# Kernel optimization log

Hardware: AMD Instinct MI355X
Metric: run time of the kernel (lower is better)

Reference implementation:

```python
import jax, jax.numpy as jnp
import numpy as np

T, B, E, H, PD, PV = 256, 64, 768, 512, 100, 1000
H2 = 2 * H


def setup_inputs() -> dict:
    key = jax.random.key(0)
    ks = jax.random.split(key, 20)
    sc_rnn = 1.0 / np.sqrt(H)
    sc_lin = 1.0 / np.sqrt(H2)
    n = lambda k, shape, s: (jax.random.normal(k, shape, jnp.float32) * s)
    return {
        "emb": n(ks[0], (T, B, E), 1.0),
        "lengths": jnp.full((B,), T, dtype=jnp.int32),
        # bidirectional LSTM params (PyTorch gate order i,f,g,o); b = b_ih + b_hh
        "w_ih_f": n(ks[1], (4 * H, E), sc_rnn),
        "w_hh_f": n(ks[2], (4 * H, H), sc_rnn),
        "b_f": n(ks[3], (4 * H,), sc_rnn),
        "w_ih_b": n(ks[4], (4 * H, E), sc_rnn),
        "w_hh_b": n(ks[5], (4 * H, H), sc_rnn),
        "b_b": n(ks[6], (4 * H,), sc_rnn),
        "W_fdoc": n(ks[7], (H2, H2), sc_lin),
        "b_fdoc": n(ks[8], (H2,), sc_lin),
        "pos_emb": n(ks[9], (PV, PD), 1.0),
        "w_content": n(ks[10], (H2,), sc_lin),
        "W_sal": n(ks[11], (H2, H2), sc_lin),
        "W_nov": n(ks[12], (H2, H2), sc_lin),
        "w_abs": n(ks[13], (PD,), 1.0 / np.sqrt(PD)),
        "bias": n(ks[14], (), 0.05),
    }


def _lstm_dir(x, w_ih, w_hh, b, reverse):
    # x: [T, B, E]; batch_first=True in the original means dim0 (T) is batch
    # and dim1 (B) is the scan (sequence) axis.
    pre = jnp.einsum('tbe,ge->tbg', x, w_ih) + b  # [T, B, 4H]
    if reverse:
        pre = pre[:, ::-1]
    pre_s = jnp.swapaxes(pre, 0, 1)  # [B, T, 4H] -> scan over B

    def step(carry, p):
        h, c = carry
        g = p + h @ w_hh.T
        i, f, gg, o = jnp.split(g, 4, axis=-1)
        c = jax.nn.sigmoid(f) * c + jax.nn.sigmoid(i) * jnp.tanh(gg)
        h = jax.nn.sigmoid(o) * jnp.tanh(c)
        return (h, c), h

    init = (jnp.zeros((x.shape[0], w_hh.shape[1]), x.dtype),
            jnp.zeros((x.shape[0], w_hh.shape[1]), x.dtype))
    _, hs = jax.lax.scan(step, init, pre_s)  # [B, T, H]
    hs = jnp.swapaxes(hs, 0, 1)  # [T, B, H]
    if reverse:
        hs = hs[:, ::-1]
    return hs


def reference(emb, lengths, w_ih_f, w_hh_f, b_f, w_ih_b, w_hh_b, b_b,
              W_fdoc, b_fdoc, pos_emb, w_content, W_sal, W_nov, w_abs, bias):
    # lengths are assumed full (= T) for static shapes under jit.
    del lengths
    fwd = _lstm_dir(emb, w_ih_f, w_hh_f, b_f, reverse=False)
    bwd = _lstm_dir(emb, w_ih_b, w_hh_b, b_b, reverse=True)
    sents = jnp.concatenate([fwd, bwd], axis=-1)  # [T, B, 2H]

    hsd = jnp.swapaxes(sents, 0, 1)  # [B, T, 2H] per-document hidden states
    doc = jnp.tanh(hsd.mean(axis=1) @ W_fdoc.T + b_fdoc)  # [B, 2H]

    cont = hsd @ w_content                                  # [B, T]
    sal = jnp.einsum('bth,hk,bk->bt', hsd, W_sal, doc)      # [B, T]
    abs_p = pos_emb[jnp.minimum(jnp.arange(T), PV - 1)] @ w_abs  # [T]
    s0 = cont + sal + abs_p[None, :] + bias                 # [B, T]

    # sequential summary recurrence over sentence positions, batched over docs
    xs = (jnp.swapaxes(hsd, 0, 1), s0.T)  # ([T,B,2H], [T,B])

    def step(summ, x):
        h, s = x
        nov = jnp.einsum('bh,hk,bk->b', h, W_nov, jnp.tanh(summ))
        prob = jax.nn.sigmoid(s - nov)
        summ = summ + prob[:, None] * h
        return summ, prob

    _, probs = jax.lax.scan(step, jnp.zeros((B, H2), emb.dtype), xs)  # [T, B]
    # original concatenates doc-by-doc, position-major within each doc
    return probs.T.reshape(-1)  # [B*T]
```

## Files before the change

### kernel.cpp

```cpp
#include <hip/hip_runtime.h>


typedef _Float16 f16x8 __attribute__((ext_vector_type(8)));
typedef float f32x4 __attribute__((ext_vector_type(4)));
typedef unsigned short us4 __attribute__((ext_vector_type(4)));
typedef unsigned short us8 __attribute__((ext_vector_type(8)));
typedef unsigned int u32x4 __attribute__((ext_vector_type(4)));

#define DEV __device__ __forceinline__

DEV unsigned short f2h(float f) {
  _Float16 h = (_Float16)f;
  return __builtin_bit_cast(unsigned short, h);
}
DEV float h2f(unsigned short u) {
  return (float)__builtin_bit_cast(_Float16, u);
}
DEV float sigf(float x) { return 1.f / (1.f + __expf(-x)); }
DEV float tanhf_(float x) { return 1.f - 2.f / (__expf(2.f * x) + 1.f); }

DEV void store_b64_llc(unsigned short* addr, us4 v) {
  asm volatile("global_store_dwordx2 %0, %1, off sc0 sc1" ::"v"(addr), "v"(v)
               : "memory");
}
DEV void waitcnt_vm0() { asm volatile("s_waitcnt vmcnt(0)" ::: "memory"); }

DEV void load_frags16_llc(const unsigned short* base, f16x8 af[16]) {
  asm volatile(
      "global_load_dwordx4 %0, %16, off sc0 sc1\n\t"
      "global_load_dwordx4 %1, %16, off offset:64 sc0 sc1\n\t"
      "global_load_dwordx4 %2, %16, off offset:128 sc0 sc1\n\t"
      "global_load_dwordx4 %3, %16, off offset:192 sc0 sc1\n\t"
      "global_load_dwordx4 %4, %16, off offset:256 sc0 sc1\n\t"
      "global_load_dwordx4 %5, %16, off offset:320 sc0 sc1\n\t"
      "global_load_dwordx4 %6, %16, off offset:384 sc0 sc1\n\t"
      "global_load_dwordx4 %7, %16, off offset:448 sc0 sc1\n\t"
      "global_load_dwordx4 %8, %16, off offset:512 sc0 sc1\n\t"
      "global_load_dwordx4 %9, %16, off offset:576 sc0 sc1\n\t"
      "global_load_dwordx4 %10, %16, off offset:640 sc0 sc1\n\t"
      "global_load_dwordx4 %11, %16, off offset:704 sc0 sc1\n\t"
      "global_load_dwordx4 %12, %16, off offset:768 sc0 sc1\n\t"
      "global_load_dwordx4 %13, %16, off offset:832 sc0 sc1\n\t"
      "global_load_dwordx4 %14, %16, off offset:896 sc0 sc1\n\t"
      "global_load_dwordx4 %15, %16, off offset:960 sc0 sc1\n\t"
      "s_waitcnt vmcnt(0)"
      : "=v"(af[0]), "=v"(af[1]), "=v"(af[2]), "=v"(af[3]), "=v"(af[4]),
        "=v"(af[5]), "=v"(af[6]), "=v"(af[7]), "=v"(af[8]), "=v"(af[9]),
        "=v"(af[10]), "=v"(af[11]), "=v"(af[12]), "=v"(af[13]), "=v"(af[14]),
        "=v"(af[15])
      : "v"(base)
      : "memory");
}

DEV void cvt4seg(const float* __restrict__ src, unsigned short* __restrict__ dst,
                 size_t nquads, size_t gt, size_t NT) {
  const f32x4* s4 = (const f32x4*)src;
  us4* d4 = (us4*)dst;
  for (size_t i = gt; i < nquads; i += NT) {
    f32x4 v = s4[i];
    us4 o = {f2h(v[0]), f2h(v[1]), f2h(v[2]), f2h(v[3])};
    d4[i] = o;
  }
}

__global__ __launch_bounds__(256, 1) void prep_kernel(
    const float* __restrict__ emb, const float* __restrict__ wihf,
    const float* __restrict__ whhf, const float* __restrict__ bf_,
    const float* __restrict__ wihb, const float* __restrict__ whhb,
    const float* __restrict__ bb_, const float* __restrict__ posemb,
    const float* __restrict__ Wnov, const float* __restrict__ wabs,
    unsigned short* __restrict__ emb_t, unsigned short* __restrict__ wcat,
    unsigned short* __restrict__ whh, unsigned short* __restrict__ WnT,
    float* __restrict__ bcat, float* __restrict__ absp,
    unsigned short* __restrict__ hst, int* __restrict__ cnt) {
  size_t gt = (size_t)blockIdx.x * 256 + threadIdx.x;
  size_t NT = (size_t)gridDim.x * 256;
  for (size_t i = gt; i < 3145728u; i += NT) {
    size_t r = i / 192, e4 = i % 192;
    size_t b = r >> 8, t = r & 255;
    f32x4 v = *(const f32x4*)(emb + (t * 64 + b) * 768 + e4 * 4);
    us4 o = {f2h(v[0]), f2h(v[1]), f2h(v[2]), f2h(v[3])};
    ((us4*)emb_t)[i] = o;
  }
  cvt4seg(wihf, wcat, 393216u, gt, NT);
  cvt4seg(wihb, wcat + 1572864, 393216u, gt, NT);
  cvt4seg(whhf, whh, 262144u, gt, NT);
  cvt4seg(whhb, whh + 1048576, 262144u, gt, NT);
  for (size_t i = gt; i < 1048576u; i += NT) {
    size_t k = i >> 10, h = i & 1023;
    WnT[i] = f2h(Wnov[h * 1024 + k]);
  }
  for (size_t i = gt; i < 4096u; i += NT)
    bcat[i] = (i < 2048) ? bf_[i] : bb_[i - 2048];
  for (size_t i = gt; i < 256u; i += NT) {
    float a = 0.f;
    for (int p = 0; p < 100; ++p) a += posemb[i * 100 + p] * wabs[p];
    absp[i] = a;
  }
  u32x4 z = {0u, 0u, 0u, 0u};
  for (size_t i = gt; i < 65536u; i += NT) ((u32x4*)hst)[i] = z;
  for (size_t i = gt; i < 2048u; i += NT) cnt[i] = 0;
}

template <int BIAS, int OF16>
__global__ __launch_bounds__(256, 2) void gemm_bt(
    const unsigned short* __restrict__ A, const unsigned short* __restrict__ B,
    void* __restrict__ C, const float* __restrict__ bias, int M, int N, int K) {
  __shared__ __align__(16) unsigned short As[128 * 32];
  __shared__ __align__(16) unsigned short Bs[128 * 32];
  const int tid = threadIdx.x;
  const size_t m0 = (size_t)blockIdx.x * 128, n0 = (size_t)blockIdx.y * 128;
  const int w = tid >> 6, l = tid & 63;
  const int rh = (w >> 1) * 64, ch = (w & 1) * 64;
  const int lm = l >> 4, ln = l & 15;
  f32x4 acc[4][4] = {};
  us8 pa[2], pb[2];
#pragma unroll
  for (int p = 0; p < 2; ++p) {
    int idx = p * 256 + tid, row = idx >> 2, kq = idx & 3;
    pa[p] = *(const us8*)(A + (m0 + row) * (size_t)K + kq * 8);
    pb[p] = *(const us8*)(B + (n0 + row) * (size_t)K + kq * 8);
  }
  for (int k0 = 0; k0 < K; k0 += 32) {
    __syncthreads();
#pragma unroll
    for (int p = 0; p < 2; ++p) {
      int idx = p * 256 + tid;
      *(us8*)&As[idx * 8] = pa[p];
      *(us8*)&Bs[idx * 8] = pb[p];
    }
    __syncthreads();
    if (k0 + 32 < K) {
#pragma unroll
      for (int p = 0; p < 2; ++p) {
        int idx = p * 256 + tid, row = idx >> 2, kq = idx & 3;
        pa[p] = *(const us8*)(A + (m0 + row) * (size_t)K + (k0 + 32) + kq * 8);
        pb[p] = *(const us8*)(B + (n0 + row) * (size_t)K + (k0 + 32) + kq * 8);
      }
    }
    f16x8 af[4], bfv[4];
#pragma unroll
    for (int r = 0; r < 4; ++r)
      af[r] = *(const f16x8*)&As[(rh + r * 16 + ln) * 32 + lm * 8];
#pragma unroll
    for (int c = 0; c < 4; ++c)
      bfv[c] = *(const f16x8*)&Bs[(ch + c * 16 + ln) * 32 + lm * 8];
#pragma unroll
    for (int r = 0; r < 4; ++r)
#pragma unroll
      for (int c = 0; c < 4; ++c)
        acc[r][c] =
            __builtin_amdgcn_mfma_f32_16x16x32_f16(af[r], bfv[c], acc[r][c], 0, 0, 0);
  }
#pragma unroll
  for (int r = 0; r < 4; ++r) {
#pragma unroll
    for (int reg = 0; reg < 4; ++reg) {
      size_t rowg = m0 + rh + r * 16 + lm * 4 + reg;
      float bv = BIAS ? bias[rowg] : 0.f;
#pragma unroll
      for (int c = 0; c < 4; ++c) {
        size_t col = n0 + ch + c * 16 + ln;
        float v = acc[r][c][reg] + bv;
        if (OF16)
          ((unsigned short*)C)[rowg * N + col] = f2h(v);
        else
          ((float*)C)[rowg * N + col] = v;
      }
    }
  }
}

__global__ __launch_bounds__(256, 1) void lstm_kernel(
    const unsigned short* __restrict__ whh,
    const unsigned short* __restrict__ pre,
    unsigned short* __restrict__ hst,
    unsigned short* __restrict__ hsd,
    int* __restrict__ cnt) {
  const int wg = blockIdx.x;
  const int d = wg >> 7;
  const int sub = wg & 127;
  const int ts = sub >> 6;
  const int s = sub & 63;
  const int u0 = s * 8;
  const int tid = threadIdx.x, wv = tid >> 6, l = tid & 63;
  const int lm = l >> 4, ln = l & 15;
  __shared__ __align__(16) float gbuf[4][32 * 33];

  f16x8 wf[2][16];
#pragma unroll
  for (int c = 0; c < 2; ++c) {
    int n = c * 16 + ln;
    const unsigned short* wrow =
        whh + ((size_t)d * 2048 + (size_t)(n >> 3) * 512 + u0 + (n & 7)) * 512;
#pragma unroll
    for (int kc = 0; kc < 16; ++kc)
      wf[c][kc] = *(const f16x8*)(wrow + kc * 32 + lm * 8);
  }
  float cst[4] = {0.f, 0.f, 0.f, 0.f};
  int* flags = cnt + (d * 2 + ts) * 64;
  const int chain0 = ts * 128 + wv * 32;

  for (int step = 0; step < 64; ++step) {
    const int b_eff = d ? (63 - step) : step;
    us4 pv[2][2];
#pragma unroll
    for (int mt = 0; mt < 2; ++mt)
#pragma unroll
      for (int c = 0; c < 2; ++c) {
        int n = c * 16 + ln;
        pv[mt][c] = *(const us4*)(pre +
            ((size_t)d * 2048 + (size_t)(n >> 3) * 512 + u0 + (n & 7)) * 16384 +
            b_eff * 256 + chain0 + mt * 16 + lm * 4);
      }
    if (step > 0) {
      if (wv == 0) {
        for (;;) {
          int v = __hip_atomic_load(flags + l, __ATOMIC_RELAXED,
                                    __HIP_MEMORY_SCOPE_AGENT);
          if (__ballot(v < step) == 0ull) break;
          __builtin_amdgcn_s_sleep(1);
        }
      }
      __syncthreads();
    }
    float pvf[2][2][4];
#pragma unroll
    for (int mt = 0; mt < 2; ++mt)
#pragma unroll
      for (int c = 0; c < 2; ++c)
#pragma unroll
        for (int reg = 0; reg < 4; ++reg) pvf[mt][c][reg] = h2f(pv[mt][c][reg]);

    const unsigned short* hbase =
        hst + ((size_t)d * 2 + (step & 1)) * (256 * 512);
#pragma unroll
    for (int mt = 0; mt < 2; ++mt) {
      f16x8 af[16];
      load_frags16_llc(hbase + (size_t)(chain0 + mt * 16 + ln) * 512 + lm * 8,
                       af);
      f32x4 a0 = {}, a1 = {};
#pragma unroll
      for (int kc = 0; kc < 16; ++kc) {
        a0 = __builtin_amdgcn_mfma_f32_16x16x32_f16(af[kc], wf[0][kc], a0, 0, 0, 0);
        a1 = __builtin_amdgcn_mfma_f32_16x16x32_f16(af[kc], wf[1][kc], a1, 0, 0, 0);
      }
#pragma unroll
      for (int c = 0; c < 2; ++c) {
        int n = c * 16 + ln;
        f32x4 A = c ? a1 : a0;
#pragma unroll
        for (int reg = 0; reg < 4; ++reg)
          gbuf[wv][(mt * 16 + lm * 4 + reg) * 33 + n] =
              A[reg] + pvf[mt][c][reg];
      }
    }
    us4 hv;
    const int t = chain0 + (l >> 1);
    {
      const float* gb = &gbuf[wv][(l >> 1) * 33];
      const int ug = (l & 1) * 4;
#pragma unroll
      for (int j = 0; j < 4; ++j) {
        int du = ug + j;
        float gi = gb[du];
        float gf = gb[8 + du];
        float gg = gb[16 + du];
        float go = gb[24 + du];
        float cn = sigf(gf) * cst[j] + sigf(gi) * tanhf_(gg);
        cst[j] = cn;
        hv[j] = f2h(sigf(go) * tanhf_(cn));
      }
      store_b64_llc(hst + ((size_t)d * 2 + ((step & 1) ^ 1)) * (256 * 512) +
                        (size_t)t * 512 + u0 + ug,
                    hv);
    }
    waitcnt_vm0();
    __syncthreads();
    if (tid == 0)
      __hip_atomic_store(flags + s, step + 1, __ATOMIC_RELAXED,
                         __HIP_MEMORY_SCOPE_AGENT);
    *(us4*)(hsd + ((size_t)(b_eff * 256 + t)) * 1024 + d * 512 + u0 +
            (l & 1) * 4) = hv;
  }
}

__global__ __launch_bounds__(256, 1) void hsum_kernel(
    const unsigned short* __restrict__ hsd, float* __restrict__ hsum) {
  int b = blockIdx.x, tid = threadIdx.x;
  const unsigned short* base = hsd + (size_t)b * 256 * 1024 + tid * 4;
  f32x4 acc = {};
  for (int t = 0; t < 256; ++t) {
    us4 v = *(const us4*)(base + t * 1024);
    acc[0] += h2f(v[0]);
    acc[1] += h2f(v[1]);
    acc[2] += h2f(v[2]);
    acc[3] += h2f(v[3]);
  }
  *(f32x4*)(hsum + (size_t)b * 1024 + tid * 4) = acc;
}

__global__ __launch_bounds__(256, 1) void rowdot_kernel(
    const float* __restrict__ W, const float* __restrict__ x,
    const float* __restrict__ bias, float* __restrict__ y, float scale,
    int do_tanh) {
  int gt = blockIdx.x * 256 + threadIdx.x;
  int b = gt >> 10, k = gt & 1023;
  const f32x4* wr = (const f32x4*)(W + (size_t)k * 1024);
  const f32x4* xr = (const f32x4*)(x + (size_t)b * 1024);
  float acc = 0.f;
  for (int j = 0; j < 256; ++j) {
    f32x4 wv = wr[j], xv = xr[j];
    acc += wv[0] * xv[0] + wv[1] * xv[1] + wv[2] * xv[2] + wv[3] * xv[3];
  }
  acc = acc * scale + (bias ? bias[k] : 0.f);
  y[gt] = do_tanh ? tanhf_(acc) : acc;
}

__global__ __launch_bounds__(256, 1) void s0_kernel(
    const unsigned short* __restrict__ hsd, const float* __restrict__ wcont,
    const float* __restrict__ d2, const float* __restrict__ absp,
    const float* __restrict__ biasp, float* __restrict__ s0) {
  int tid = threadIdx.x, wv = tid >> 6, l = tid & 63;
  int idx = blockIdx.x * 4 + wv;
  int b = idx >> 8, t = idx & 255;
  const unsigned short* hr = hsd + (size_t)idx * 1024 + l * 16;
  const float* wc = wcont + l * 16;
  const float* dr = d2 + (size_t)b * 1024 + l * 16;
  float sc = 0.f, ss = 0.f;
#pragma unroll
  for (int j = 0; j < 16; ++j) {
    float hf = h2f(hr[j]);
    sc += hf * wc[j];
    ss += hf * dr[j];
  }
#pragma unroll
  for (int off = 32; off; off >>= 1) {
    sc += __shfl_down(sc, off);
    ss += __shfl_down(ss, off);
  }
  if (l == 0) s0[idx] = sc + ss + absp[t] + biasp[0];
}

__global__ __launch_bounds__(256, 1) void scan_kernel(
    const float* __restrict__ Anov, const unsigned short* __restrict__ hsd,
    const float* __restrict__ s0, float* __restrict__ out) {
  int b = blockIdx.x, tid = threadIdx.x, wv = tid >> 6, l = tid & 63;
  __shared__ float red[4];
  float summ[4] = {0.f, 0.f, 0.f, 0.f};
  const float* Ab = Anov + (size_t)b * 256 * 1024 + tid * 4;
  const unsigned short* hb = hsd + (size_t)b * 256 * 1024 + tid * 4;
  const float* sb = s0 + b * 256;
  float* ob = out + b * 256;
  f32x4 a = *(const f32x4*)Ab;
  us4 hv = *(const us4*)hb;
  for (int t = 0; t < 256; ++t) {
    f32x4 ac = a;
    us4 hc = hv;
    if (t < 255) {
      a = *(const f32x4*)(Ab + (t + 1) * 1024);
      hv = *(const us4*)(hb + (t + 1) * 1024);
    }
    float p = ac[0] * tanhf_(summ[0]) + ac[1] * tanhf_(summ[1]) +
              ac[2] * tanhf_(summ[2]) + ac[3] * tanhf_(summ[3]);
#pragma unroll
    for (int off = 32; off; off >>= 1) p += __shfl_down(p, off);
    if (l == 0) red[wv] = p;
    __syncthreads();
    float nov = red[0] + red[1] + red[2] + red[3];
    float prob = sigf(sb[t] - nov);
    summ[0] += prob * h2f(hc[0]);
    summ[1] += prob * h2f(hc[1]);
    summ[2] += prob * h2f(hc[2]);
    summ[3] += prob * h2f(hc[3]);
    if (tid == 0) ob[t] = prob;
    __syncthreads();
  }
}

extern "C" void kernel_launch(void* const* d_in, const int* in_sizes, int n_in,
                              void* d_out, int out_size, void* d_ws,
                              size_t ws_size, hipStream_t stream) {
  const float* emb = (const float*)d_in[0];
  const float* wihf = (const float*)d_in[2];
  const float* whhf = (const float*)d_in[3];
  const float* bf_ = (const float*)d_in[4];
  const float* wihb = (const float*)d_in[5];
  const float* whhb = (const float*)d_in[6];
  const float* bb_ = (const float*)d_in[7];
  const float* Wfdoc = (const float*)d_in[8];
  const float* bfdoc = (const float*)d_in[9];
  const float* posemb = (const float*)d_in[10];
  const float* wcont = (const float*)d_in[11];
  const float* Wsal = (const float*)d_in[12];
  const float* Wnov = (const float*)d_in[13];
  const float* wabs = (const float*)d_in[14];
  const float* biasp = (const float*)d_in[15];

  char* ws = (char*)d_ws;
  unsigned short* PRE = (unsigned short*)(ws + 0);
  float* Anov = (float*)(ws + 0);
  unsigned short* emb_t = (unsigned short*)(ws + 134217728);
  unsigned short* wcat = (unsigned short*)(ws + 159383552);
  unsigned short* whh = (unsigned short*)(ws + 165675008);
  unsigned short* WnT = (unsigned short*)(ws + 169869312);
  unsigned short* hsd = (unsigned short*)(ws + 171966464);
  unsigned short* hst = (unsigned short*)(ws + 205520896);
  float* hsum = (float*)(ws + 206569472);
  float* doc = (float*)(ws + 206831616);
  float* d2 = (float*)(ws + 207093760);
  float* s0 = (float*)(ws + 207355904);
  float* absp = (float*)(ws + 207421440);
  float* bcat = (float*)(ws + 207422464);
  int* cnt = (int*)(ws + 207438848);
  float* out = (float*)d_out;

  prep_kernel<<<dim3(2048), dim3(256), 0, stream>>>(
      emb, wihf, whhf, bf_, wihb, whhb, bb_, posemb, Wnov, wabs, emb_t, wcat,
      whh, WnT, bcat, absp, hst, cnt);
  gemm_bt<1, 1><<<dim3(32, 128), dim3(256), 0, stream>>>(
      wcat, emb_t, (void*)PRE, bcat, 4096, 16384, 768);
  lstm_kernel<<<dim3(256), dim3(256), 0, stream>>>(whh, PRE, hst, hsd, cnt);
  hsum_kernel<<<dim3(64), dim3(256), 0, stream>>>(hsd, hsum);
  rowdot_kernel<<<dim3(256), dim3(256), 0, stream>>>(Wfdoc, hsum, bfdoc, doc,
                                                     1.f / 256.f, 1);
  rowdot_kernel<<<dim3(256), dim3(256), 0, stream>>>(Wsal, doc, (const float*)nullptr,
                                                     d2, 1.f, 0);
  s0_kernel<<<dim3(4096), dim3(256), 0, stream>>>(hsd, wcont, d2, absp, biasp, s0);
  gemm_bt<0, 0><<<dim3(128, 8), dim3(256), 0, stream>>>(
      hsd, WnT, (void*)Anov, (const float*)nullptr, 16384, 1024, 1024);
  scan_kernel<<<dim3(64), dim3(256), 0, stream>>>(Anov, hsd, s0, out);
}
```

Baseline: 1.063 ms.

## Use per-wave progress flags instead of workgroup barriers in LSTM recurrence

Each wave now publishes and polls its own completion flag across the 64 column-slice workgroups, so the two __syncthreads per step are removed and waves advance independently along their own 32-chain slice. The recurrent weight fragments are also loaded through inline asm with early-clobber outputs, which appears intended to keep them pinned in registers, and the existing fragment loader gets early-clobber constraints too. The flag array grows fourfold, so the host-side flag buffer must be sized and zeroed to match. Every wave now spins on global atomics, which raises polling traffic.

```diff
diff --git a/kernel.cpp b/kernel.cpp
--- a/kernel.cpp
+++ b/kernel.cpp
@@ -44,10 +44,37 @@
       "global_load_dwordx4 %14, %16, off offset:896 sc0 sc1\n\t"
       "global_load_dwordx4 %15, %16, off offset:960 sc0 sc1\n\t"
       "s_waitcnt vmcnt(0)"
-      : "=v"(af[0]), "=v"(af[1]), "=v"(af[2]), "=v"(af[3]), "=v"(af[4]),
-        "=v"(af[5]), "=v"(af[6]), "=v"(af[7]), "=v"(af[8]), "=v"(af[9]),
-        "=v"(af[10]), "=v"(af[11]), "=v"(af[12]), "=v"(af[13]), "=v"(af[14]),
-        "=v"(af[15])
+      : "=&v"(af[0]), "=&v"(af[1]), "=&v"(af[2]), "=&v"(af[3]), "=&v"(af[4]),
+        "=&v"(af[5]), "=&v"(af[6]), "=&v"(af[7]), "=&v"(af[8]), "=&v"(af[9]),
+        "=&v"(af[10]), "=&v"(af[11]), "=&v"(af[12]), "=&v"(af[13]),
+        "=&v"(af[14]), "=&v"(af[15])
+      : "v"(base)
+      : "memory");
+}
+
+DEV void load_frags16_pin(const unsigned short* base, f16x8 wf[16]) {
+  asm volatile(
+      "global_load_dwordx4 %0, %16, off\n\t"
+      "global_load_dwordx4 %1, %16, off offset:64\n\t"
+      "global_load_dwordx4 %2, %16, off offset:128\n\t"
+      "global_load_dwordx4 %3, %16, off offset:192\n\t"
+      "global_load_dwordx4 %4, %16, off offset:256\n\t"
+      "global_load_dwordx4 %5, %16, off offset:320\n\t"
+      "global_load_dwordx4 %6, %16, off offset:384\n\t"
+      "global_load_dwordx4 %7, %16, off offset:448\n\t"
+      "global_load_dwordx4 %8, %16, off offset:512\n\t"
+      "global_load_dwordx4 %9, %16, off offset:576\n\t"
+      "global_load_dwordx4 %10, %16, off offset:640\n\t"
+      "global_load_dwordx4 %11, %16, off offset:704\n\t"
+      "global_load_dwordx4 %12, %16, off offset:768\n\t"
+      "global_load_dwordx4 %13, %16, off offset:832\n\t"
+      "global_load_dwordx4 %14, %16, off offset:896\n\t"
+      "global_load_dwordx4 %15, %16, off offset:960\n\t"
+      "s_waitcnt vmcnt(0)"
+      : "=&v"(wf[0]), "=&v"(wf[1]), "=&v"(wf[2]), "=&v"(wf[3]), "=&v"(wf[4]),
+        "=&v"(wf[5]), "=&v"(wf[6]), "=&v"(wf[7]), "=&v"(wf[8]), "=&v"(wf[9]),
+        "=&v"(wf[10]), "=&v"(wf[11]), "=&v"(wf[12]), "=&v"(wf[13]),
+        "=&v"(wf[14]), "=&v"(wf[15])
       : "v"(base)
       : "memory");
 }
@@ -187,18 +214,20 @@
   const int lm = l >> 4, ln = l & 15;
   __shared__ __align__(16) float gbuf[4][32 * 33];
 
-  f16x8 wf[2][16];
-#pragma unroll
-  for (int c = 0; c < 2; ++c) {
-    int n = c * 16 + ln;
-    const unsigned short* wrow =
-        whh + ((size_t)d * 2048 + (size_t)(n >> 3) * 512 + u0 + (n & 7)) * 512;
-#pragma unroll
-    for (int kc = 0; kc < 16; ++kc)
-      wf[c][kc] = *(const f16x8*)(wrow + kc * 32 + lm * 8);
+  f16x8 wf0[16], wf1[16];
+  {
+    const int na = ln, nb = 16 + ln;
+    load_frags16_pin(
+        whh + ((size_t)d * 2048 + (size_t)(na >> 3) * 512 + u0 + (na & 7)) * 512 +
+            lm * 8,
+        wf0);
+    load_frags16_pin(
+        whh + ((size_t)d * 2048 + (size_t)(nb >> 3) * 512 + u0 + (nb & 7)) * 512 +
+            lm * 8,
+        wf1);
   }
   float cst[4] = {0.f, 0.f, 0.f, 0.f};
-  int* flags = cnt + (d * 2 + ts) * 64;
+  int* flags = cnt + ((d * 2 + ts) * 4 + wv) * 64;
   const int chain0 = ts * 128 + wv * 32;
 
   for (int step = 0; step < 64; ++step) {
@@ -214,15 +243,12 @@
             b_eff * 256 + chain0 + mt * 16 + lm * 4);
       }
     if (step > 0) {
-      if (wv == 0) {
-        for (;;) {
-          int v = __hip_atomic_load(flags + l, __ATOMIC_RELAXED,
-                                    __HIP_MEMORY_SCOPE_AGENT);
-          if (__ballot(v < step) == 0ull) break;
-          __builtin_amdgcn_s_sleep(1);
-        }
-      }
-      __syncthreads();
+      for (;;) {
+        int v = __hip_atomic_load(flags + l, __ATOMIC_RELAXED,
+                                  __HIP_MEMORY_SCOPE_AGENT);
+        if (__ballot(v < step) == 0ull) break;
+        __builtin_amdgcn_s_sleep(1);
+      }
     }
     float pvf[2][2][4];
 #pragma unroll
@@ -242,8 +268,8 @@
       f32x4 a0 = {}, a1 = {};
 #pragma unroll
       for (int kc = 0; kc < 16; ++kc) {
-        a0 = __builtin_amdgcn_mfma_f32_16x16x32_f16(af[kc], wf[0][kc], a0, 0, 0, 0);
-        a1 = __builtin_amdgcn_mfma_f32_16x16x32_f16(af[kc], wf[1][kc], a1, 0, 0, 0);
+        a0 = __builtin_amdgcn_mfma_f32_16x16x32_f16(af[kc], wf0[kc], a0, 0, 0, 0);
+        a1 = __builtin_amdgcn_mfma_f32_16x16x32_f16(af[kc], wf1[kc], a1, 0, 0, 0);
       }
 #pragma unroll
       for (int c = 0; c < 2; ++c) {
@@ -276,8 +302,7 @@
                     hv);
     }
     waitcnt_vm0();
-    __syncthreads();
-    if (tid == 0)
+    if (l == 0)
       __hip_atomic_store(flags + s, step + 1, __ATOMIC_RELAXED,
                          __HIP_MEMORY_SCOPE_AGENT);
     *(us4*)(hsd + ((size_t)(b_eff * 256 + t)) * 1024 + d * 512 + u0 +
```

Result: slower. 1.282 ms (+20.6%).
